# Kernel optimization log

Hardware: AMD Instinct MI355X
Metric: run time of the kernel (lower is better)

The kernel has to match this reference:

```python
import jax, jax.numpy as jnp
import numpy as np

B, M, N = 4, 2048, 2048


def setup_inputs() -> dict:
    key = jax.random.key(0)
    x = jax.random.normal(key, (B, M, N), dtype=jnp.float32)
    return {"x": x}


def _cos_mat(n):
    # C[u, k] = cos(pi * (2u+1) * k / (2n))  -- IDXCT basis (full x_0 term, no halving)
    u = jnp.arange(n, dtype=jnp.float32)
    k = jnp.arange(n, dtype=jnp.float32)
    return jnp.cos((jnp.pi / (2.0 * n)) * (2.0 * u[:, None] + 1.0) * k[None, :])


def _sin_mat(n):
    # S[u, k] = sin(pi * (2u+1) * k / (2n))  -- IDXST basis (k=0 term vanishes)
    u = jnp.arange(n, dtype=jnp.float32)
    k = jnp.arange(n, dtype=jnp.float32)
    return jnp.sin((jnp.pi / (2.0 * n)) * (2.0 * u[:, None] + 1.0) * k[None, :])


def reference(x):
    """idsct2(x) = idxst(idxct(x)^T)^T

    out[b, u, v] = sum_{p, q} x[b, p, q] * sin(pi*(2u+1)*p/(2M)) * cos(pi*(2v+1)*q/(2N))

    The original dispatches to an O(n log n) FFT-butterfly CUDA/C++ kernel; the
    math it computes is this separable cosine/sine transform, expressed here as
    two dense contractions (the clean O(n^2)-per-axis reference form).
    """
    m, n = x.shape[-2], x.shape[-1]
    C = _cos_mat(n)  # [v, q]
    S = _sin_mat(m)  # [u, p]
    t = jnp.einsum('bpq,vq->bpv', x, C)   # idxct along the last dim
    out = jnp.einsum('up,bpv->buv', S, t)  # idxst along the second-to-last dim
    return out
```

## Files before the change

kernel.cpp:

```cpp
#include <hip/hip_runtime.h>
#include <hip/hip_bf16.h>
#include <math.h>


#define BM 128
#define BN 256
#define BK 32
#define KDIM 1024

typedef __bf16 bf16x8 __attribute__((ext_vector_type(8)));
typedef __bf16 bf16x4 __attribute__((ext_vector_type(4)));
typedef float floatx4 __attribute__((ext_vector_type(4)));

__device__ __forceinline__ void async_ld16(const void* g, void* l) {
    __builtin_amdgcn_global_load_lds(
        (__attribute__((address_space(1))) void*)(g),
        (__attribute__((address_space(3))) void*)(l), 16, 0, 0);
}

#define BARX() __builtin_amdgcn_s_barrier()
#define VM6() asm volatile("s_waitcnt vmcnt(6)" ::: "memory")
#define VM0() asm volatile("s_waitcnt vmcnt(0)" ::: "memory")
#define NOPSTMT ((void)0)

__global__ void prep_kernel(const float4* __restrict__ x,
                            bf16x4* __restrict__ xe, bf16x4* __restrict__ xo,
                            __bf16* __restrict__ Ce, __bf16* __restrict__ Co,
                            __bf16* __restrict__ Se, __bf16* __restrict__ So) {
    int b = blockIdx.x;
    if (b < 4096) {
        int idx = b * 256 + threadIdx.x;
        int vp = idx >> 10;
        int j = idx & 1023;
        int pe = ((2 * vp + 1) * (2 * j)) & 8191;
        int po = ((2 * vp + 1) * (2 * j + 1)) & 8191;
        float ae = (float)pe * 7.669903939428206e-04f;
        float ao = (float)po * 7.669903939428206e-04f;
        float se, ce, so, co;
        __sincosf(ae, &se, &ce);
        __sincosf(ao, &so, &co);
        Ce[idx] = (__bf16)ce;
        Co[idx] = (__bf16)co;
        Se[idx] = (__bf16)se;
        So[idx] = (__bf16)so;
    } else {
        int g = (b - 4096) * 256 + threadIdx.x;
        float4 v0 = x[2 * g];
        float4 v1 = x[2 * g + 1];
        bf16x4 e, o;
        e[0] = (__bf16)v0.x; e[1] = (__bf16)v0.z;
        e[2] = (__bf16)v1.x; e[3] = (__bf16)v1.z;
        o[0] = (__bf16)v0.y; o[1] = (__bf16)v0.w;
        o[2] = (__bf16)v1.y; o[3] = (__bf16)v1.w;
        xe[g] = e;
        xo[g] = o;
    }
}

template <int PASS>
__global__ void __launch_bounds__(512, 2) gemm_eo(
    const __bf16* __restrict__ Ae, const __bf16* __restrict__ Ao,
    const __bf16* __restrict__ Be, const __bf16* __restrict__ Bo,
    __bf16* __restrict__ D0, __bf16* __restrict__ D1,
    float* __restrict__ Df) {
    __shared__ __bf16 lds[3][24576];
    constexpr int OFF_AE = 0, OFF_AO = 4096, OFF_BE = 8192, OFF_BO = 16384;

    const int tid = threadIdx.x;
    const int lane = tid & 63;
    const int wave = tid >> 6;
    const int wr = wave >> 2;
    const int wc = wave & 3;

    const size_t zB = (size_t)blockIdx.z * 2048 * 1024;
    Be += zB; Bo += zB;

    const int row0 = blockIdx.y * BM;
    const int col0 = blockIdx.x * BN;

    const int srow = tid >> 2;
    const int scs = tid & 3;
    const int sgc = (scs ^ ((srow >> 1) & 3)) * 8;
    const __bf16* aeS = Ae + (size_t)(row0 + srow) * KDIM + sgc;
    const __bf16* aoS = Ao + (size_t)(row0 + srow) * KDIM + sgc;
    const __bf16* beS = Be + (size_t)(col0 + srow) * KDIM + sgc;
    const __bf16* boS = Bo + (size_t)(col0 + srow) * KDIM + sgc;
    const int ldsW = wave << 9;

    auto STG_E = [&](int s, int kt) {
        async_ld16(aeS + kt * BK, &lds[s][OFF_AE + ldsW]);
        async_ld16(beS + kt * BK, &lds[s][OFF_BE + ldsW]);
        async_ld16(beS + kt * BK + (size_t)128 * KDIM,
                   &lds[s][OFF_BE + 4096 + ldsW]);
    };
    auto STG_O = [&](int s, int kt) {
        async_ld16(aoS + kt * BK, &lds[s][OFF_AO + ldsW]);
        async_ld16(boS + kt * BK, &lds[s][OFF_BO + ldsW]);
        async_ld16(boS + kt * BK + (size_t)128 * KDIM,
                   &lds[s][OFF_BO + 4096 + ldsW]);
    };

    const int fr = lane & 15;
    const int fc = lane >> 4;
    const int slotOff = (fc ^ ((fr >> 1) & 3)) * 8;
    const int aBase = (wr * 64 + fr) * BK + slotOff;
    const int bBase = (wc * 64 + fr) * BK + slotOff;

    bf16x8 afrE[4], bfrE[4], afrO[4], bfrO[4];
    floatx4 accE[4][4] = {};
    floatx4 accO[4][4] = {};

    auto LDF = [&](const __bf16* buf, int aOff, int bOff,
                   bf16x8(&af)[4], bf16x8(&bf)[4]) {
#pragma unroll
        for (int i = 0; i < 4; ++i)
            af[i] = *(const bf16x8*)&buf[aOff + aBase + i * 16 * BK];
#pragma unroll
        for (int j = 0; j < 4; ++j)
            bf[j] = *(const bf16x8*)&buf[bOff + bBase + j * 16 * BK];
    };
    auto MMA16 = [&](floatx4(&acc)[4][4], bf16x8(&af)[4], bf16x8(&bf)[4]) {
        __builtin_amdgcn_s_setprio(1);
#pragma unroll
        for (int i = 0; i < 4; ++i)
#pragma unroll
            for (int j = 0; j < 4; ++j)
                acc[i][j] = __builtin_amdgcn_mfma_f32_16x16x32_bf16(
                    af[i], bf[j], acc[i][j], 0, 0, 0);
        __builtin_amdgcn_s_setprio(0);
    };

#define TILE(bc, SE, SO, VMW) do {                              \
        LDF(lds[bc], OFF_AE, OFF_BE, afrE, bfrE);               \
        LDF(lds[bc], OFF_AO, OFF_BO, afrO, bfrO);               \
        SE; SO;                                                 \
        MMA16(accE, afrE, bfrE);                                \
        MMA16(accO, afrO, bfrO);                                \
        VMW; BARX();                                            \
    } while (0)

    STG_E(0, 0); STG_O(0, 0);
    STG_E(1, 1); STG_O(1, 1);
    VM6();
    BARX();

    for (int i = 0; i < 10; ++i) {
        const int t = 3 * i;
        TILE(0, STG_E(2, t + 2), STG_O(2, t + 2), VM6());
        TILE(1, STG_E(0, t + 3), STG_O(0, t + 3), VM6());
        TILE(2, STG_E(1, t + 4), STG_O(1, t + 4), VM6());
    }
    TILE(0, NOPSTMT, NOPSTMT, VM0());
    TILE(1, NOPSTMT, NOPSTMT, NOPSTMT);
#undef TILE

    const int ecol = lane & 15;
    const int erow = (lane >> 4) * 4;
#pragma unroll
    for (int i = 0; i < 4; ++i)
#pragma unroll
        for (int j = 0; j < 4; ++j)
#pragma unroll
            for (int r = 0; r < 4; ++r) {
                const int gi = row0 + wr * 64 + i * 16 + erow + r;
                const int gj = col0 + wc * 64 + j * 16 + ecol;
                const float e = accE[i][j][r];
                const float o = accO[i][j][r];
                if (PASS == 1) {
                    __bf16* base = (gj & 1) ? D1 : D0;
                    base += zB;
                    const size_t m = (size_t)(gj >> 1);
                    base[(size_t)gi * 1024 + m] = (__bf16)(e + o);
                    base[(size_t)(2047 - gi) * 1024 + m] = (__bf16)(e - o);
                } else {
                    float* ob = Df + (size_t)blockIdx.z * 2048 * 2048;
                    ob[(size_t)gi * 2048 + gj] = e + o;
                    ob[(size_t)(2047 - gi) * 2048 + gj] = o - e;
                }
            }
}

extern "C" void kernel_launch(void* const* d_in, const int* in_sizes, int n_in,
                              void* d_out, int out_size, void* d_ws, size_t ws_size,
                              hipStream_t stream) {
    const float* x = (const float*)d_in[0];
    float* out = (float*)d_out;

    const size_t m1 = (size_t)1024 * 1024;
    const size_t hm = (size_t)4 * 2048 * 1024;

    __bf16* Ce = (__bf16*)d_ws;
    __bf16* Co = Ce + m1;
    __bf16* Se = Co + m1;
    __bf16* So = Se + m1;
    __bf16* xe = So + m1;
    __bf16* xo = xe + hm;
    __bf16* tTe = xo + hm;
    __bf16* tTo = tTe + hm;

    prep_kernel<<<12288, 256, 0, stream>>>((const float4*)x, (bf16x4*)xe,
                                           (bf16x4*)xo, Ce, Co, Se, So);

    dim3 grid(2048 / BN, 1024 / BM, 4);
    gemm_eo<1><<<grid, 512, 0, stream>>>(Ce, Co, xe, xo, tTe, tTo, nullptr);
    gemm_eo<2><<<grid, 512, 0, stream>>>(Se, So, tTe, tTo, nullptr, nullptr, out);
}
```

Baseline: 192.3 us.

## Split even/odd GEMMs across wave groups with smaller tiles and LDS reduction

The block tile shrinks from 128x256 to 128x128. The eight waves now split into two groups: one computes the even-part product and the other the odd-part product, each holding a single 4x4 accumulator set. This replaces the old scheme where every wave held both sets. The pipeline goes from triple to double buffering with an extra barrier per tile. The odd accumulators are handed to the even waves through a swizzled LDS exchange before the symmetric epilogue. The goal is lower register pressure and higher occupancy (launch bounds raised to 4 blocks per SM), at the cost of more barriers, a shallower prefetch, and the LDS exchange step.

```diff
diff --git a/kernel.cpp b/kernel.cpp
--- a/kernel.cpp
+++ b/kernel.cpp
@@ -4,7 +4,7 @@
 
 
 #define BM 128
-#define BN 256
+#define BN 128
 #define BK 32
 #define KDIM 1024
 
@@ -19,7 +19,7 @@
 }
 
 #define BARX() __builtin_amdgcn_s_barrier()
-#define VM6() asm volatile("s_waitcnt vmcnt(6)" ::: "memory")
+#define VM4() asm volatile("s_waitcnt vmcnt(4)" ::: "memory")
 #define VM0() asm volatile("s_waitcnt vmcnt(0)" ::: "memory")
 #define NOPSTMT ((void)0)
 
@@ -58,19 +58,20 @@
 }
 
 template <int PASS>
-__global__ void __launch_bounds__(512, 2) gemm_eo(
+__global__ void __launch_bounds__(512, 4) gemm_eo(
     const __bf16* __restrict__ Ae, const __bf16* __restrict__ Ao,
     const __bf16* __restrict__ Be, const __bf16* __restrict__ Bo,
     __bf16* __restrict__ D0, __bf16* __restrict__ D1,
     float* __restrict__ Df) {
-    __shared__ __bf16 lds[3][24576];
-    constexpr int OFF_AE = 0, OFF_AO = 4096, OFF_BE = 8192, OFF_BO = 16384;
+    __shared__ __bf16 lds[2][16384];
+    constexpr int OFF_AE = 0, OFF_AO = 4096, OFF_BE = 8192, OFF_BO = 12288;
 
     const int tid = threadIdx.x;
     const int lane = tid & 63;
     const int wave = tid >> 6;
-    const int wr = wave >> 2;
-    const int wc = wave & 3;
+    const int par = wave >> 2;
+    const int wr = (wave >> 1) & 1;
+    const int wc = wave & 1;
 
     const size_t zB = (size_t)blockIdx.z * 2048 * 1024;
     Be += zB; Bo += zB;
@@ -78,48 +79,40 @@
     const int row0 = blockIdx.y * BM;
     const int col0 = blockIdx.x * BN;
 
-    const int srow = tid >> 2;
-    const int scs = tid & 3;
-    const int sgc = (scs ^ ((srow >> 1) & 3)) * 8;
+    const int srow = wave * 16 + (lane >> 2);
+    const int sgc = ((lane & 3) ^ ((lane >> 3) & 3)) * 8;
     const __bf16* aeS = Ae + (size_t)(row0 + srow) * KDIM + sgc;
     const __bf16* aoS = Ao + (size_t)(row0 + srow) * KDIM + sgc;
     const __bf16* beS = Be + (size_t)(col0 + srow) * KDIM + sgc;
     const __bf16* boS = Bo + (size_t)(col0 + srow) * KDIM + sgc;
     const int ldsW = wave << 9;
 
-    auto STG_E = [&](int s, int kt) {
-        async_ld16(aeS + kt * BK, &lds[s][OFF_AE + ldsW]);
-        async_ld16(beS + kt * BK, &lds[s][OFF_BE + ldsW]);
-        async_ld16(beS + kt * BK + (size_t)128 * KDIM,
-                   &lds[s][OFF_BE + 4096 + ldsW]);
-    };
-    auto STG_O = [&](int s, int kt) {
-        async_ld16(aoS + kt * BK, &lds[s][OFF_AO + ldsW]);
-        async_ld16(boS + kt * BK, &lds[s][OFF_BO + ldsW]);
-        async_ld16(boS + kt * BK + (size_t)128 * KDIM,
-                   &lds[s][OFF_BO + 4096 + ldsW]);
+    auto STG = [&](int s, int kt) {
+        const size_t ko = (size_t)kt * BK;
+        async_ld16(aeS + ko, &lds[s][OFF_AE + ldsW]);
+        async_ld16(aoS + ko, &lds[s][OFF_AO + ldsW]);
+        async_ld16(beS + ko, &lds[s][OFF_BE + ldsW]);
+        async_ld16(boS + ko, &lds[s][OFF_BO + ldsW]);
     };
 
     const int fr = lane & 15;
     const int fc = lane >> 4;
     const int slotOff = (fc ^ ((fr >> 1) & 3)) * 8;
-    const int aBase = (wr * 64 + fr) * BK + slotOff;
-    const int bBase = (wc * 64 + fr) * BK + slotOff;
-
-    bf16x8 afrE[4], bfrE[4], afrO[4], bfrO[4];
-    floatx4 accE[4][4] = {};
-    floatx4 accO[4][4] = {};
-
-    auto LDF = [&](const __bf16* buf, int aOff, int bOff,
-                   bf16x8(&af)[4], bf16x8(&bf)[4]) {
-#pragma unroll
-        for (int i = 0; i < 4; ++i)
-            af[i] = *(const bf16x8*)&buf[aOff + aBase + i * 16 * BK];
+    const int aBase = (par ? OFF_AO : OFF_AE) + (wr * 64 + fr) * BK + slotOff;
+    const int bBase = (par ? OFF_BO : OFF_BE) + (wc * 64 + fr) * BK + slotOff;
+
+    bf16x8 af[4], bf[4];
+    floatx4 acc[4][4] = {};
+
+    auto LDF = [&](int buf) {
+#pragma unroll
+        for (int i = 0; i < 4; ++i)
+            af[i] = *(const bf16x8*)&lds[buf][aBase + i * 16 * BK];
 #pragma unroll
         for (int j = 0; j < 4; ++j)
-            bf[j] = *(const bf16x8*)&buf[bOff + bBase + j * 16 * BK];
+            bf[j] = *(const bf16x8*)&lds[buf][bBase + j * 16 * BK];
     };
-    auto MMA16 = [&](floatx4(&acc)[4][4], bf16x8(&af)[4], bf16x8(&bf)[4]) {
+    auto MMA16 = [&]() {
         __builtin_amdgcn_s_setprio(1);
 #pragma unroll
         for (int i = 0; i < 4; ++i)
@@ -130,54 +123,67 @@
         __builtin_amdgcn_s_setprio(0);
     };
 
-#define TILE(bc, SE, SO, VMW) do {                              \
-        LDF(lds[bc], OFF_AE, OFF_BE, afrE, bfrE);               \
-        LDF(lds[bc], OFF_AO, OFF_BO, afrO, bfrO);               \
-        SE; SO;                                                 \
-        MMA16(accE, afrE, bfrE);                                \
-        MMA16(accO, afrO, bfrO);                                \
-        VMW; BARX();                                            \
+#define TILE(bc, SG, VMW) do {          \
+        LDF(bc); MMA16(); BARX();       \
+        SG; VMW; BARX();                \
     } while (0)
 
-    STG_E(0, 0); STG_O(0, 0);
-    STG_E(1, 1); STG_O(1, 1);
-    VM6();
+    STG(0, 0); STG(1, 1);
+    VM4();
     BARX();
 
-    for (int i = 0; i < 10; ++i) {
-        const int t = 3 * i;
-        TILE(0, STG_E(2, t + 2), STG_O(2, t + 2), VM6());
-        TILE(1, STG_E(0, t + 3), STG_O(0, t + 3), VM6());
-        TILE(2, STG_E(1, t + 4), STG_O(1, t + 4), VM6());
-    }
-    TILE(0, NOPSTMT, NOPSTMT, VM0());
-    TILE(1, NOPSTMT, NOPSTMT, NOPSTMT);
+    for (int i = 0; i < 15; ++i) {
+        const int t = 2 * i;
+        TILE(0, STG(0, t + 2), VM4());
+        TILE(1, STG(1, t + 3), VM4());
+    }
+    TILE(0, NOPSTMT, VM0());
+    TILE(1, NOPSTMT, NOPSTMT);
 #undef TILE
 
+    float* ldsF = (float*)&lds[0][0];
     const int ecol = lane & 15;
     const int erow = (lane >> 4) * 4;
-#pragma unroll
-    for (int i = 0; i < 4; ++i)
-#pragma unroll
-        for (int j = 0; j < 4; ++j)
-#pragma unroll
-            for (int r = 0; r < 4; ++r) {
-                const int gi = row0 + wr * 64 + i * 16 + erow + r;
-                const int gj = col0 + wc * 64 + j * 16 + ecol;
-                const float e = accE[i][j][r];
-                const float o = accO[i][j][r];
-                if (PASS == 1) {
-                    __bf16* base = (gj & 1) ? D1 : D0;
-                    base += zB;
-                    const size_t m = (size_t)(gj >> 1);
-                    base[(size_t)gi * 1024 + m] = (__bf16)(e + o);
-                    base[(size_t)(2047 - gi) * 1024 + m] = (__bf16)(e - o);
-                } else {
-                    float* ob = Df + (size_t)blockIdx.z * 2048 * 2048;
-                    ob[(size_t)gi * 2048 + gj] = e + o;
-                    ob[(size_t)(2047 - gi) * 2048 + gj] = o - e;
+    if (par == 1) {
+#pragma unroll
+        for (int i = 0; i < 4; ++i)
+#pragma unroll
+            for (int j = 0; j < 4; ++j) {
+                const int li0 = wr * 64 + i * 16 + erow;
+                const int lj = wc * 64 + j * 16 + ecol;
+                *(floatx4*)&ldsF[lj * 128 + (li0 ^ ((lj & 7) << 3))] = acc[i][j];
+            }
+    }
+    __syncthreads();
+    if (par == 0) {
+#pragma unroll
+        for (int i = 0; i < 4; ++i)
+#pragma unroll
+            for (int j = 0; j < 4; ++j) {
+                const int li0 = wr * 64 + i * 16 + erow;
+                const int lj = wc * 64 + j * 16 + ecol;
+                const floatx4 o4 =
+                    *(const floatx4*)&ldsF[lj * 128 + (li0 ^ ((lj & 7) << 3))];
+#pragma unroll
+                for (int r = 0; r < 4; ++r) {
+                    const int gi = row0 + li0 + r;
+                    const int gj = col0 + lj;
+                    const float e = acc[i][j][r];
+                    const float o = o4[r];
+                    if (PASS == 1) {
+                        __bf16* base = (gj & 1) ? D1 : D0;
+                        base += zB;
+                        const size_t m = (size_t)(gj >> 1);
+                        base[(size_t)gi * 1024 + m] = (__bf16)(e + o);
+                        base[(size_t)(2047 - gi) * 1024 + m] = (__bf16)(e - o);
+                    } else {
+                        float* ob = Df + (size_t)blockIdx.z * 2048 * 2048;
+                        ob[(size_t)gi * 2048 + gj] = e + o;
+                        ob[(size_t)(2047 - gi) * 2048 + gj] = o - e;
+                    }
                 }
             }
+    }
 }
 
 extern "C" void kernel_launch(void* const* d_in, const int* in_sizes, int n_in,
```

After: 205.9 us. 1.07x slower.

## Load B fragments directly from global into registers, shrink LDS to double buffer

Applied to the files above, without the earlier changes.

The B operand (x or intermediate) is no longer staged through LDS. Each wave loads its B fragments straight from global memory into registers, double-buffered in registers, while only the A operand (cos/sin basis) goes through async LDS loads with two buffers instead of three. The goal is to cut LDS footprint and LDS read traffic, and possibly raise occupancy. The cost is redundant global loads of B across the two wave rows, uncoalesced 16-byte strided reads, much higher register pressure from four extra fragment arrays, and a vmcnt(8) wait that mixes register loads with LDS-bound async loads.

```diff
diff --git a/kernel.cpp b/kernel.cpp
--- a/kernel.cpp
+++ b/kernel.cpp
@@ -19,9 +19,7 @@
 }
 
 #define BARX() __builtin_amdgcn_s_barrier()
-#define VM6() asm volatile("s_waitcnt vmcnt(6)" ::: "memory")
-#define VM0() asm volatile("s_waitcnt vmcnt(0)" ::: "memory")
-#define NOPSTMT ((void)0)
+#define VM8() asm volatile("s_waitcnt vmcnt(8)" ::: "memory")
 
 __global__ void prep_kernel(const float4* __restrict__ x,
                             bf16x4* __restrict__ xe, bf16x4* __restrict__ xo,
@@ -63,8 +61,8 @@
     const __bf16* __restrict__ Be, const __bf16* __restrict__ Bo,
     __bf16* __restrict__ D0, __bf16* __restrict__ D1,
     float* __restrict__ Df) {
-    __shared__ __bf16 lds[3][24576];
-    constexpr int OFF_AE = 0, OFF_AO = 4096, OFF_BE = 8192, OFF_BO = 16384;
+    __shared__ __bf16 lds[2][8192];
+    constexpr int OFF_AE = 0, OFF_AO = 4096;
 
     const int tid = threadIdx.x;
     const int lane = tid & 63;
@@ -79,45 +77,35 @@
     const int col0 = blockIdx.x * BN;
 
     const int srow = tid >> 2;
-    const int scs = tid & 3;
-    const int sgc = (scs ^ ((srow >> 1) & 3)) * 8;
+    const int sgc = ((tid & 3) ^ ((srow >> 1) & 3)) * 8;
     const __bf16* aeS = Ae + (size_t)(row0 + srow) * KDIM + sgc;
     const __bf16* aoS = Ao + (size_t)(row0 + srow) * KDIM + sgc;
-    const __bf16* beS = Be + (size_t)(col0 + srow) * KDIM + sgc;
-    const __bf16* boS = Bo + (size_t)(col0 + srow) * KDIM + sgc;
     const int ldsW = wave << 9;
 
-    auto STG_E = [&](int s, int kt) {
+    auto STG = [&](int s, int kt) {
         async_ld16(aeS + kt * BK, &lds[s][OFF_AE + ldsW]);
-        async_ld16(beS + kt * BK, &lds[s][OFF_BE + ldsW]);
-        async_ld16(beS + kt * BK + (size_t)128 * KDIM,
-                   &lds[s][OFF_BE + 4096 + ldsW]);
-    };
-    auto STG_O = [&](int s, int kt) {
         async_ld16(aoS + kt * BK, &lds[s][OFF_AO + ldsW]);
-        async_ld16(boS + kt * BK, &lds[s][OFF_BO + ldsW]);
-        async_ld16(boS + kt * BK + (size_t)128 * KDIM,
-                   &lds[s][OFF_BO + 4096 + ldsW]);
     };
 
     const int fr = lane & 15;
     const int fc = lane >> 4;
     const int slotOff = (fc ^ ((fr >> 1) & 3)) * 8;
     const int aBase = (wr * 64 + fr) * BK + slotOff;
-    const int bBase = (wc * 64 + fr) * BK + slotOff;
-
-    bf16x8 afrE[4], bfrE[4], afrO[4], bfrO[4];
+
+    const __bf16* bE = Be + (size_t)(col0 + wc * 64 + fr) * KDIM + fc * 8;
+    const __bf16* bO = Bo + (size_t)(col0 + wc * 64 + fr) * KDIM + fc * 8;
+
+    bf16x8 afE[4], afO[4];
+    bf16x8 bfE0[4], bfO0[4], bfE1[4], bfO1[4];
     floatx4 accE[4][4] = {};
     floatx4 accO[4][4] = {};
 
-    auto LDF = [&](const __bf16* buf, int aOff, int bOff,
-                   bf16x8(&af)[4], bf16x8(&bf)[4]) {
-#pragma unroll
-        for (int i = 0; i < 4; ++i)
-            af[i] = *(const bf16x8*)&buf[aOff + aBase + i * 16 * BK];
-#pragma unroll
-        for (int j = 0; j < 4; ++j)
-            bf[j] = *(const bf16x8*)&buf[bOff + bBase + j * 16 * BK];
+    auto LDF = [&](int buf) {
+#pragma unroll
+        for (int i = 0; i < 4; ++i) {
+            afE[i] = *(const bf16x8*)&lds[buf][OFF_AE + aBase + i * 16 * BK];
+            afO[i] = *(const bf16x8*)&lds[buf][OFF_AO + aBase + i * 16 * BK];
+        }
     };
     auto MMA16 = [&](floatx4(&acc)[4][4], bf16x8(&af)[4], bf16x8(&bf)[4]) {
         __builtin_amdgcn_s_setprio(1);
@@ -130,29 +118,41 @@
         __builtin_amdgcn_s_setprio(0);
     };
 
-#define TILE(bc, SE, SO, VMW) do {                              \
-        LDF(lds[bc], OFF_AE, OFF_BE, afrE, bfrE);               \
-        LDF(lds[bc], OFF_AO, OFF_BO, afrO, bfrO);               \
-        SE; SO;                                                 \
-        MMA16(accE, afrE, bfrE);                                \
-        MMA16(accO, afrO, bfrO);                                \
-        VMW; BARX();                                            \
+#define LDB(n, kt)                                                          \
+    do {                                                                    \
+        _Pragma("unroll")                                                   \
+        for (int j = 0; j < 4; ++j) {                                       \
+            bfE##n[j] = *(const bf16x8*)&bE[(size_t)j * 16 * KDIM + (kt) * BK]; \
+            bfO##n[j] = *(const bf16x8*)&bO[(size_t)j * 16 * KDIM + (kt) * BK]; \
+        }                                                                   \
     } while (0)
 
-    STG_E(0, 0); STG_O(0, 0);
-    STG_E(1, 1); STG_O(1, 1);
-    VM6();
+#define TILE(c, n, kt1)                           \
+    do {                                          \
+        STG(n, kt1);                              \
+        LDB(n, kt1);                              \
+        LDF(c);                                   \
+        MMA16(accE, afE, bfE##c);                 \
+        MMA16(accO, afO, bfO##c);                 \
+        VM8();                                    \
+        BARX();                                   \
+    } while (0)
+
+    STG(0, 0);
+    LDB(0, 0);
+    VM8();
     BARX();
 
-    for (int i = 0; i < 10; ++i) {
-        const int t = 3 * i;
-        TILE(0, STG_E(2, t + 2), STG_O(2, t + 2), VM6());
-        TILE(1, STG_E(0, t + 3), STG_O(0, t + 3), VM6());
-        TILE(2, STG_E(1, t + 4), STG_O(1, t + 4), VM6());
+    for (int i = 0; i < 15; ++i) {
+        TILE(0, 1, 2 * i + 1);
+        TILE(1, 0, 2 * i + 2);
     }
-    TILE(0, NOPSTMT, NOPSTMT, VM0());
-    TILE(1, NOPSTMT, NOPSTMT, NOPSTMT);
+    TILE(0, 1, 31);
+    LDF(1);
+    MMA16(accE, afE, bfE1);
+    MMA16(accO, afO, bfO1);
 #undef TILE
+#undef LDB
 
     const int ecol = lane & 15;
     const int erow = (lane >> 4) * 4;
```

New measurement: 274.1 us. +42.5%, slower.
